# Kernel optimization log

Measured on AMD Instinct MI355X. Metric: run time of the kernel, lower is better.

The kernel has to match this reference:

```python
import jax, jax.numpy as jnp
import numpy as np

TEMPERATURE = 0.07


def setup_inputs() -> dict:
    key = jax.random.key(0)
    k1, k2 = jax.random.split(key)
    B, D = 8192, 128
    z_i = jax.random.normal(k1, (B, D), dtype=jnp.float32)
    z_j = jax.random.normal(k2, (B, D), dtype=jnp.float32)
    return {"z_i": z_i, "z_j": z_j}


def reference(z_i, z_j):
    B = z_i.shape[0]
    # L2-normalize each embedding (F.normalize with eps=1e-12 clamp)
    def l2norm(x):
        n = jnp.linalg.norm(x, axis=1, keepdims=True)
        return x / jnp.maximum(n, 1e-12)
    reps = jnp.concatenate([l2norm(z_i), l2norm(z_j)], axis=0)  # [2B, D]
    sim = jnp.matmul(reps, reps.T) / TEMPERATURE  # [2B, 2B]
    # NOTE: original code applies CrossEntropyLoss to exp(sim/T) values,
    # i.e. the logits themselves are the exponentiated similarities.
    e = jnp.exp(sim)
    N = 2 * B
    idx = jnp.arange(N)
    # CE with the positive placed first and all non-diagonal entries as logits:
    # loss_i = logsumexp(nondiag row) - positive_logit
    neg_inf = jnp.asarray(-jnp.inf, dtype=e.dtype)
    row_logits = jnp.where(idx[None, :] == idx[:, None], neg_inf, e)  # mask diagonal
    lse = jax.scipy.special.logsumexp(row_logits, axis=1)  # [2B]
    pos_idx = jnp.where(idx < B, idx + B, idx - B)
    pos = e[idx, pos_idx]  # [2B]
    return jnp.mean(lse - pos)
```

## Files before the change

kernel.cpp:

```cpp
#include <hip/hip_runtime.h>
#include <hip/hip_bf16.h>


#define NROWS 16384
#define BHALF 8192
#define DDIM  128
#define TILE  128
#define ROWS_PER_BLOCK 256
#define NSPLIT 8
#define COLS_PER_SPLIT (NROWS / NSPLIT)
#define NITERS (COLS_PER_SPLIT / TILE)
#define LDS_STRIDE 136
#define LOG2E 1.4426950408889634f
#define C_EXP (LOG2E / 0.07f)
#define NEGBIG -1.0e30f

typedef __attribute__((ext_vector_type(8))) short bf16x8;
typedef __attribute__((ext_vector_type(4))) float f32x4;

__device__ inline unsigned short f2bf(float x) {
    unsigned int b = __float_as_uint(x);
    b += 0x7FFFu + ((b >> 16) & 1u);
    return (unsigned short)(b >> 16);
}
__device__ inline float bflo(unsigned int u) { return __uint_as_float(u << 16); }
__device__ inline float bfhi(unsigned int u) { return __uint_as_float(u & 0xFFFF0000u); }

__global__ void norm_kernel(const float* __restrict__ zi, const float* __restrict__ zj,
                            unsigned short* __restrict__ repsB,
                            unsigned short* __restrict__ repsA,
                            float* __restrict__ out) {
    int w = threadIdx.x >> 6;
    int lane = threadIdx.x & 63;
    int row = blockIdx.x * 4 + w;
    const float* src = (row < BHALF) ? (zi + (size_t)row * DDIM)
                                     : (zj + (size_t)(row - BHALF) * DDIM);
    float2 v = ((const float2*)src)[lane];
    float ss = v.x * v.x + v.y * v.y;
    #pragma unroll
    for (int d = 1; d < 64; d <<= 1) ss += __shfl_xor(ss, d, 64);
    float inv = 1.0f / fmaxf(sqrtf(ss), 1e-12f);
    float x = v.x * inv, y = v.y * inv;
    unsigned int pb = (unsigned int)f2bf(x) | ((unsigned int)f2bf(y) << 16);
    unsigned int pa = (unsigned int)f2bf(x * C_EXP) | ((unsigned int)f2bf(y * C_EXP) << 16);
    ((unsigned int*)repsB)[(size_t)row * (DDIM / 2) + lane] = pb;
    ((unsigned int*)repsA)[(size_t)row * (DDIM / 2) + lane] = pa;
    if (blockIdx.x == 0 && threadIdx.x == 0) out[0] = 0.0f;
}

template <bool DIAG>
__device__ __forceinline__ void tile_compute(const unsigned short* __restrict__ lds,
                                             const bf16x8 (&afrag)[4][4],
                                             float (&A1)[4][4], float (&A2)[4][4],
                                             int rowBase, int colBase,
                                             int laneLo, int quad) {
    #pragma unroll
    for (int c8 = 0; c8 < 8; ++c8) {
        bf16x8 bfrag[4];
        int brow = c8 * 16 + laneLo;
        #pragma unroll
        for (int kt = 0; kt < 4; ++kt)
            bfrag[kt] = *(const bf16x8*)(&lds[brow * LDS_STRIDE + kt * 32 + quad * 8]);
        #pragma unroll
        for (int rt = 0; rt < 4; ++rt) {
            f32x4 acc = (f32x4){0.f, 0.f, 0.f, 0.f};
            #pragma unroll
            for (int kt = 0; kt < 4; ++kt)
                acc = __builtin_amdgcn_mfma_f32_16x16x32_bf16(
                    afrag[rt][kt], bfrag[kt], acc, 0, 0, 0);
            #pragma unroll
            for (int rg = 0; rg < 4; ++rg) {
                float a = acc[rg];
                if (DIAG) {
                    int drel = rowBase + rt * 16 + quad * 4 + rg - colBase - laneLo;
                    a = (drel == c8 * 16) ? NEGBIG : a;
                }
                float mn = fminf(a, A1[rt][rg]);
                A2[rt][rg] = fmaxf(A2[rt][rg], mn);
                A1[rt][rg] = fmaxf(A1[rt][rg], a);
            }
        }
    }
}

__global__ __launch_bounds__(256, 2)
void ntx_main(const unsigned short* __restrict__ repsA,
              const unsigned short* __restrict__ repsB,
              float2* __restrict__ part) {
    __shared__ unsigned short lds[2][TILE * LDS_STRIDE];
    const int tid = threadIdx.x;
    const int w = tid >> 6, lane = tid & 63;
    const int laneLo = lane & 15, quad = lane >> 4;
    const int bx = blockIdx.x, by = blockIdx.y;
    const int rowBase = bx * ROWS_PER_BLOCK + w * 64;

    bf16x8 afrag[4][4];
    #pragma unroll
    for (int rt = 0; rt < 4; ++rt)
        #pragma unroll
        for (int kt = 0; kt < 4; ++kt) {
            int r = rowBase + rt * 16 + laneLo;
            int k = kt * 32 + quad * 8;
            afrag[rt][kt] = *(const bf16x8*)(repsA + (size_t)r * DDIM + k);
        }

    float A1[4][4], A2[4][4];
    #pragma unroll
    for (int rt = 0; rt < 4; ++rt)
        #pragma unroll
        for (int rg = 0; rg < 4; ++rg) { A1[rt][rg] = NEGBIG; A2[rt][rg] = NEGBIG; }

    const int colBase0 = by * COLS_PER_SPLIT;
    const uint4* repsV = (const uint4*)repsB;
    const int r0 = tid >> 4, c0 = tid & 15;

    uint4 pf[8];
    #pragma unroll
    for (int i = 0; i < 8; ++i)
        pf[i] = repsV[(size_t)(colBase0 + r0 + i * 16) * 16 + c0];
    #pragma unroll
    for (int i = 0; i < 8; ++i)
        *(uint4*)(&lds[0][(r0 + i * 16) * LDS_STRIDE + c0 * 8]) = pf[i];

    int buf = 0;
    for (int it = 0; it < NITERS; ++it) {
        __syncthreads();
        int colBase = colBase0 + it * TILE;
        int nextCol = colBase0 + ((it + 1) & (NITERS - 1)) * TILE;
        #pragma unroll
        for (int i = 0; i < 8; ++i)
            pf[i] = repsV[(size_t)(nextCol + r0 + i * 16) * 16 + c0];

        if ((rowBase >> 7) == (colBase >> 7))
            tile_compute<true>(lds[buf], afrag, A1, A2, rowBase, colBase, laneLo, quad);
        else
            tile_compute<false>(lds[buf], afrag, A1, A2, rowBase, colBase, laneLo, quad);

        #pragma unroll
        for (int i = 0; i < 8; ++i)
            *(uint4*)(&lds[buf ^ 1][(r0 + i * 16) * LDS_STRIDE + c0 * 8]) = pf[i];
        buf ^= 1;
    }

    #pragma unroll
    for (int rt = 0; rt < 4; ++rt)
        #pragma unroll
        for (int rg = 0; rg < 4; ++rg) {
            float m1 = A1[rt][rg], m2 = A2[rt][rg];
            #pragma unroll
            for (int d = 1; d < 16; d <<= 1) {
                float m1o = __shfl_xor(m1, d, 64);
                float m2o = __shfl_xor(m2, d, 64);
                m2 = fmaxf(fmaxf(m2, m2o), fminf(m1, m1o));
                m1 = fmaxf(m1, m1o);
            }
            if (laneLo == 0) {
                int gr = rowBase + rt * 16 + quad * 4 + rg;
                part[(size_t)gr * NSPLIT + by] = make_float2(m1, m2);
            }
        }
}

__global__ void finish_kernel(const unsigned short* __restrict__ repsB,
                              const float2* __restrict__ part,
                              float* __restrict__ out) {
    int row = blockIdx.x * 256 + threadIdx.x;
    int prow = (row < BHALF) ? row + BHALF : row - BHALF;
    const uint4* rv = (const uint4*)repsB + (size_t)row * 16;
    const uint4* pv = (const uint4*)repsB + (size_t)prow * 16;
    float dot = 0.0f;
    #pragma unroll
    for (int c = 0; c < 16; ++c) {
        uint4 a = rv[c], b = pv[c];
        dot = fmaf(bflo(a.x), bflo(b.x), dot); dot = fmaf(bfhi(a.x), bfhi(b.x), dot);
        dot = fmaf(bflo(a.y), bflo(b.y), dot); dot = fmaf(bfhi(a.y), bfhi(b.y), dot);
        dot = fmaf(bflo(a.z), bflo(b.z), dot); dot = fmaf(bfhi(a.z), bfhi(b.z), dot);
        dot = fmaf(bflo(a.w), bflo(b.w), dot); dot = fmaf(bfhi(a.w), bfhi(b.w), dot);
    }
    float pos = __builtin_amdgcn_exp2f(dot * C_EXP);

    float M1 = NEGBIG, M2 = NEGBIG;
    #pragma unroll
    for (int k = 0; k < NSPLIT; ++k) {
        float2 p = part[(size_t)row * NSPLIT + k];
        M2 = fmaxf(fmaxf(M2, p.y), fminf(M1, p.x));
        M1 = fmaxf(M1, p.x);
    }
    float e1 = __builtin_amdgcn_exp2f(M1);
    float e2 = __builtin_amdgcn_exp2f(M2);
    float lse = e1 + log1pf(__builtin_amdgcn_exp2f((e2 - e1) * LOG2E));
    float v = lse - pos;

    #pragma unroll
    for (int d = 1; d < 64; d <<= 1) v += __shfl_xor(v, d, 64);
    __shared__ float red[4];
    int lane = threadIdx.x & 63, w = threadIdx.x >> 6;
    if (lane == 0) red[w] = v;
    __syncthreads();
    if (threadIdx.x == 0)
        atomicAdd(out, (red[0] + red[1] + red[2] + red[3]) * (1.0f / NROWS));
}

extern "C" void kernel_launch(void* const* d_in, const int* in_sizes, int n_in,
                              void* d_out, int out_size, void* d_ws, size_t ws_size,
                              hipStream_t stream) {
    const float* zi = (const float*)d_in[0];
    const float* zj = (const float*)d_in[1];
    float* out = (float*)d_out;
    unsigned short* repsB = (unsigned short*)d_ws;
    unsigned short* repsA = repsB + (size_t)NROWS * DDIM;
    float2* part = (float2*)((char*)d_ws + 2 * (size_t)NROWS * DDIM * 2);

    norm_kernel<<<NROWS / 4, 256, 0, stream>>>(zi, zj, repsB, repsA, out);
    ntx_main<<<dim3(NROWS / ROWS_PER_BLOCK, NSPLIT), 256, 0, stream>>>(repsA, repsB, part);
    finish_kernel<<<NROWS / 256, 256, 0, stream>>>(repsB, part, out);
}
```

Measured before the change: 137.2 us.

## Drop LDS staging for B tiles, fuse positive term into normalization

The main kernel no longer stages column tiles through double-buffered LDS with barriers. Each lane loads its MFMA B fragments straight from global memory and relies on the L1/L2 caches, and occupancy is raised to three blocks per CU. The grid is reordered so column splits vary fastest. The positive-pair logit is now computed in fp32 inside the normalization kernel, which handles the z_i and z_j rows together, so the finish kernel no longer rereads the bf16 embeddings. This removes the LDS traffic and synchronization but adds uncoalesced global loads that depend on cache hits, plus an extra memset launch.

Measured after the change: 217.4 us. 1.58x slower.

```diff
diff --git a/kernel.cpp b/kernel.cpp
--- a/kernel.cpp
+++ b/kernel.cpp
@@ -10,7 +10,6 @@
 #define NSPLIT 8
 #define COLS_PER_SPLIT (NROWS / NSPLIT)
 #define NITERS (COLS_PER_SPLIT / TILE)
-#define LDS_STRIDE 136
 #define LOG2E 1.4426950408889634f
 #define C_EXP (LOG2E / 0.07f)
 #define NEGBIG -1.0e30f
@@ -23,8 +22,9 @@
     b += 0x7FFFu + ((b >> 16) & 1u);
     return (unsigned short)(b >> 16);
 }
-__device__ inline float bflo(unsigned int u) { return __uint_as_float(u << 16); }
-__device__ inline float bfhi(unsigned int u) { return __uint_as_float(u & 0xFFFF0000u); }
+__device__ inline unsigned int pack2(float x, float y) {
+    return (unsigned int)f2bf(x) | ((unsigned int)f2bf(y) << 16);
+}
 
 __global__ void norm_kernel(const float* __restrict__ zi, const float* __restrict__ zj,
                             unsigned short* __restrict__ repsB,
@@ -32,24 +32,36 @@
                             float* __restrict__ out) {
     int w = threadIdx.x >> 6;
     int lane = threadIdx.x & 63;
-    int row = blockIdx.x * 4 + w;
-    const float* src = (row < BHALF) ? (zi + (size_t)row * DDIM)
-                                     : (zj + (size_t)(row - BHALF) * DDIM);
-    float2 v = ((const float2*)src)[lane];
-    float ss = v.x * v.x + v.y * v.y;
+    int r = blockIdx.x * 4 + w;
+    float2 a = ((const float2*)(zi + (size_t)r * DDIM))[lane];
+    float2 b = ((const float2*)(zj + (size_t)r * DDIM))[lane];
+    float si = a.x * a.x + a.y * a.y;
+    float sj = b.x * b.x + b.y * b.y;
+    float dj = a.x * b.x + a.y * b.y;
     #pragma unroll
-    for (int d = 1; d < 64; d <<= 1) ss += __shfl_xor(ss, d, 64);
-    float inv = 1.0f / fmaxf(sqrtf(ss), 1e-12f);
-    float x = v.x * inv, y = v.y * inv;
-    unsigned int pb = (unsigned int)f2bf(x) | ((unsigned int)f2bf(y) << 16);
-    unsigned int pa = (unsigned int)f2bf(x * C_EXP) | ((unsigned int)f2bf(y * C_EXP) << 16);
-    ((unsigned int*)repsB)[(size_t)row * (DDIM / 2) + lane] = pb;
-    ((unsigned int*)repsA)[(size_t)row * (DDIM / 2) + lane] = pa;
-    if (blockIdx.x == 0 && threadIdx.x == 0) out[0] = 0.0f;
+    for (int d = 1; d < 64; d <<= 1) {
+        si += __shfl_xor(si, d, 64);
+        sj += __shfl_xor(sj, d, 64);
+        dj += __shfl_xor(dj, d, 64);
+    }
+    float ii = 1.0f / fmaxf(sqrtf(si), 1e-12f);
+    float ij = 1.0f / fmaxf(sqrtf(sj), 1e-12f);
+    float xi = a.x * ii, yi = a.y * ii;
+    float xj = b.x * ij, yj = b.y * ij;
+    ((unsigned int*)repsB)[(size_t)r * (DDIM / 2) + lane] = pack2(xi, yi);
+    ((unsigned int*)repsA)[(size_t)r * (DDIM / 2) + lane] = pack2(xi * C_EXP, yi * C_EXP);
+    ((unsigned int*)repsB)[(size_t)(r + BHALF) * (DDIM / 2) + lane] = pack2(xj, yj);
+    ((unsigned int*)repsA)[(size_t)(r + BHALF) * (DDIM / 2) + lane] = pack2(xj * C_EXP, yj * C_EXP);
+
+    __shared__ float red[4];
+    if (lane == 0) red[w] = __builtin_amdgcn_exp2f(dj * ii * ij * C_EXP);
+    __syncthreads();
+    if (threadIdx.x == 0)
+        atomicAdd(out, -(red[0] + red[1] + red[2] + red[3]) * (2.0f / NROWS));
 }
 
 template <bool DIAG>
-__device__ __forceinline__ void tile_compute(const unsigned short* __restrict__ lds,
+__device__ __forceinline__ void tile_compute(const unsigned short* __restrict__ bt,
                                              const bf16x8 (&afrag)[4][4],
                                              float (&A1)[4][4], float (&A2)[4][4],
                                              int rowBase, int colBase,
@@ -57,10 +69,9 @@
     #pragma unroll
     for (int c8 = 0; c8 < 8; ++c8) {
         bf16x8 bfrag[4];
-        int brow = c8 * 16 + laneLo;
         #pragma unroll
         for (int kt = 0; kt < 4; ++kt)
-            bfrag[kt] = *(const bf16x8*)(&lds[brow * LDS_STRIDE + kt * 32 + quad * 8]);
+            bfrag[kt] = *(const bf16x8*)(bt + c8 * 16 * DDIM + kt * 32);
         #pragma unroll
         for (int rt = 0; rt < 4; ++rt) {
             f32x4 acc = (f32x4){0.f, 0.f, 0.f, 0.f};
@@ -83,15 +94,15 @@
     }
 }
 
-__global__ __launch_bounds__(256, 2)
+__global__ __launch_bounds__(256, 3)
 void ntx_main(const unsigned short* __restrict__ repsA,
               const unsigned short* __restrict__ repsB,
               float2* __restrict__ part) {
-    __shared__ unsigned short lds[2][TILE * LDS_STRIDE];
     const int tid = threadIdx.x;
     const int w = tid >> 6, lane = tid & 63;
     const int laneLo = lane & 15, quad = lane >> 4;
-    const int bx = blockIdx.x, by = blockIdx.y;
+    const int by = blockIdx.x;
+    const int bx = blockIdx.y;
     const int rowBase = bx * ROWS_PER_BLOCK + w * 64;
 
     bf16x8 afrag[4][4];
@@ -111,35 +122,15 @@
         for (int rg = 0; rg < 4; ++rg) { A1[rt][rg] = NEGBIG; A2[rt][rg] = NEGBIG; }
 
     const int colBase0 = by * COLS_PER_SPLIT;
-    const uint4* repsV = (const uint4*)repsB;
-    const int r0 = tid >> 4, c0 = tid & 15;
+    const unsigned short* bp = repsB + (size_t)(colBase0 + laneLo) * DDIM + quad * 8;
 
-    uint4 pf[8];
-    #pragma unroll
-    for (int i = 0; i < 8; ++i)
-        pf[i] = repsV[(size_t)(colBase0 + r0 + i * 16) * 16 + c0];
-    #pragma unroll
-    for (int i = 0; i < 8; ++i)
-        *(uint4*)(&lds[0][(r0 + i * 16) * LDS_STRIDE + c0 * 8]) = pf[i];
-
-    int buf = 0;
     for (int it = 0; it < NITERS; ++it) {
-        __syncthreads();
         int colBase = colBase0 + it * TILE;
-        int nextCol = colBase0 + ((it + 1) & (NITERS - 1)) * TILE;
-        #pragma unroll
-        for (int i = 0; i < 8; ++i)
-            pf[i] = repsV[(size_t)(nextCol + r0 + i * 16) * 16 + c0];
-
+        const unsigned short* bt = bp + it * (TILE * DDIM);
         if ((rowBase >> 7) == (colBase >> 7))
-            tile_compute<true>(lds[buf], afrag, A1, A2, rowBase, colBase, laneLo, quad);
+            tile_compute<true>(bt, afrag, A1, A2, rowBase, colBase, laneLo, quad);
         else
-            tile_compute<false>(lds[buf], afrag, A1, A2, rowBase, colBase, laneLo, quad);
-
-        #pragma unroll
-        for (int i = 0; i < 8; ++i)
-            *(uint4*)(&lds[buf ^ 1][(r0 + i * 16) * LDS_STRIDE + c0 * 8]) = pf[i];
-        buf ^= 1;
+            tile_compute<false>(bt, afrag, A1, A2, rowBase, colBase, laneLo, quad);
     }
 
     #pragma unroll
@@ -161,24 +152,9 @@
         }
 }
 
-__global__ void finish_kernel(const unsigned short* __restrict__ repsB,
-                              const float2* __restrict__ part,
+__global__ void finish_kernel(const float2* __restrict__ part,
                               float* __restrict__ out) {
     int row = blockIdx.x * 256 + threadIdx.x;
-    int prow = (row < BHALF) ? row + BHALF : row - BHALF;
-    const uint4* rv = (const uint4*)repsB + (size_t)row * 16;
-    const uint4* pv = (const uint4*)repsB + (size_t)prow * 16;
-    float dot = 0.0f;
-    #pragma unroll
-    for (int c = 0; c < 16; ++c) {
-        uint4 a = rv[c], b = pv[c];
-        dot = fmaf(bflo(a.x), bflo(b.x), dot); dot = fmaf(bfhi(a.x), bfhi(b.x), dot);
-        dot = fmaf(bflo(a.y), bflo(b.y), dot); dot = fmaf(bfhi(a.y), bfhi(b.y), dot);
-        dot = fmaf(bflo(a.z), bflo(b.z), dot); dot = fmaf(bfhi(a.z), bfhi(b.z), dot);
-        dot = fmaf(bflo(a.w), bflo(b.w), dot); dot = fmaf(bfhi(a.w), bfhi(b.w), dot);
-    }
-    float pos = __builtin_amdgcn_exp2f(dot * C_EXP);
-
     float M1 = NEGBIG, M2 = NEGBIG;
     #pragma unroll
     for (int k = 0; k < NSPLIT; ++k) {
@@ -188,8 +164,7 @@
     }
     float e1 = __builtin_amdgcn_exp2f(M1);
     float e2 = __builtin_amdgcn_exp2f(M2);
-    float lse = e1 + log1pf(__builtin_amdgcn_exp2f((e2 - e1) * LOG2E));
-    float v = lse - pos;
+    float v = e1 + log1pf(__builtin_amdgcn_exp2f((e2 - e1) * LOG2E));
 
     #pragma unroll
     for (int d = 1; d < 64; d <<= 1) v += __shfl_xor(v, d, 64);
@@ -211,7 +186,8 @@
     unsigned short* repsA = repsB + (size_t)NROWS * DDIM;
     float2* part = (float2*)((char*)d_ws + 2 * (size_t)NROWS * DDIM * 2);
 
-    norm_kernel<<<NROWS / 4, 256, 0, stream>>>(zi, zj, repsB, repsA, out);
-    ntx_main<<<dim3(NROWS / ROWS_PER_BLOCK, NSPLIT), 256, 0, stream>>>(repsA, repsB, part);
-    finish_kernel<<<NROWS / 256, 256, 0, stream>>>(repsB, part, out);
+    hipMemsetAsync(out, 0, sizeof(float), stream);
+    norm_kernel<<<BHALF / 4, 256, 0, stream>>>(zi, zj, repsB, repsA, out);
+    ntx_main<<<dim3(NSPLIT, NROWS / ROWS_PER_BLOCK), 256, 0, stream>>>(repsA, repsB, part);
+    finish_kernel<<<NROWS / 256, 256, 0, stream>>>(part, out);
 }
```
